# Optimization experiments

Measured on AMD Instinct MI355X. Metric: run time of the kernel, lower is better.

## Reference

```python
import jax, jax.numpy as jnp
import numpy as np

BIG = 1e10  # large finite value standing in for +inf in masked mins (grad-safe)


def setup_inputs() -> dict:
    key = jax.random.key(0)
    k1, k2, k3 = jax.random.split(key, 3)
    B, C, N = 16, 3, 4096
    x = jax.random.normal(k1, (B, C, N), dtype=jnp.float32)
    y = jax.random.normal(k2, (B, C, N), dtype=jnp.float32)
    mask = jax.random.randint(k3, (B, N), 0, 2, dtype=jnp.int32)
    return {"x": x, "y": y, "mask": mask}


def reference(x, y, mask):
    # x, y: (B, 3, N); mask: (B, N) with 1 = valid point
    xt = jnp.swapaxes(x, 1, 2)  # (B, N, 3)
    yt = jnp.swapaxes(y, 1, 2)  # (B, N, 3)
    xx = jnp.sum(xt * xt, axis=-1)  # (B, N)
    yy = jnp.sum(yt * yt, axis=-1)  # (B, N)
    # squared pairwise distances, P[b, n, m] = ||x_bn - y_bm||^2
    P = xx[:, :, None] + yy[:, None, :] - 2.0 * jnp.einsum("bnd,bmd->bnm", xt, yt)

    valid = mask.astype(bool)                 # (B, N)
    mf = mask.astype(P.dtype)                 # (B, N)
    cnt = jnp.sum(mf, axis=1)                 # (B,) number of valid points per batch

    # direction 1: for each y-point m, min over valid x-rows n; mean over valid m
    mins1 = jnp.min(jnp.where(valid[:, :, None], P, BIG), axis=1)  # (B, N)
    means1 = jnp.sum(mins1 * mf, axis=1) / cnt                      # (B,)

    # direction 2: for each x-point m, min over valid y-cols n; mean over valid m
    mins2 = jnp.min(jnp.where(valid[:, None, :], P, BIG), axis=2)  # (B, N)
    means2 = jnp.sum(mins2 * mf, axis=1) / cnt                      # (B,)

    return jnp.mean(means1) + jnp.mean(means2)
```

## Files before the change

### kernel.cpp

```cpp
#include <hip/hip_runtime.h>

typedef short bf16x8 __attribute__((ext_vector_type(8)));
typedef float f32x16 __attribute__((ext_vector_type(16)));

#define BIG_F 1e10f
constexpr int B = 16;
constexpr int N = 4096;
constexpr int ROWS = 128;
constexpr int COLS = 512;
constexpr int NRB = N / ROWS;
constexpr int NCB = N / COLS;

__device__ __forceinline__ void split(float v, unsigned& h, unsigned& l) {
    unsigned hb = __float_as_uint(v) & 0xFFFF0000u;
    h = hb >> 16;
    float r = v - __uint_as_float(hb);
    l = __float_as_uint(r) >> 16;
}

__device__ __forceinline__ float min3f(float a, float b, float c) {
    return fminf(fminf(a, b), c);
}

__device__ __forceinline__ float vmin16(f32x16 C) {
    float u0 = min3f(C[0], C[1], C[2]);
    float u1 = min3f(C[3], C[4], C[5]);
    float u2 = min3f(C[6], C[7], C[8]);
    float u3 = min3f(C[9], C[10], C[11]);
    float u4 = min3f(C[12], C[13], C[14]);
    return min3f(min3f(u0, u1, u2), fminf(u3, u4), C[15]);
}

__global__ __launch_bounds__(256) void pack_kernel(
    const float* __restrict__ x, const float* __restrict__ y,
    const int* __restrict__ mask,
    uint4* __restrict__ Apg,
    uint4* __restrict__ Bpg,
    float* __restrict__ out)
{
    const int idx = blockIdx.x * 256 + threadIdx.x;
    if (idx == 0) out[0] = 0.0f;
    const int b  = idx >> 12;
    const int pt = idx & (N - 1);
    const float* xb = x + (size_t)b * 3 * N;
    const float* yb = y + (size_t)b * 3 * N;
    const float madd = mask[b * N + pt] ? 0.0f : BIG_F;
    {
        float x0 = xb[pt], x1 = xb[N + pt], x2 = xb[2 * N + pt];
        float xx = fmaf(x2, x2, fmaf(x1, x1, x0 * x0)) + madd;
        unsigned h0, l0, h1, l1, h2, l2, xh, xl;
        split(-2.0f * x0, h0, l0);
        split(-2.0f * x1, h1, l1);
        split(-2.0f * x2, h2, l2);
        split(xx, xh, xl);
        uint4 w0 = { h0 | (h1 << 16), h2 | (h0 << 16), h1 | (h2 << 16), l0 | (l1 << 16) };
        uint4 w1 = { l2 | (l0 << 16), l1 | (l2 << 16), xh | (xl << 16), 0x3F803F80u };
        Apg[(size_t)(b * 2 + 0) * N + pt] = w0;
        Apg[(size_t)(b * 2 + 1) * N + pt] = w1;
    }
    {
        float y0 = yb[pt], y1 = yb[N + pt], y2 = yb[2 * N + pt];
        float yy = fmaf(y2, y2, fmaf(y1, y1, y0 * y0)) + madd;
        unsigned h0, l0, h1, l1, h2, l2, qh, ql;
        split(y0, h0, l0);
        split(y1, h1, l1);
        split(y2, h2, l2);
        split(yy, qh, ql);
        unsigned u0 = h0 | (h1 << 16);
        unsigned u1 = h2 | (l0 << 16);
        unsigned u2 = l1 | (l2 << 16);
        uint4 w0 = { u0, u1, u2, u0 };
        uint4 w1 = { u1, u2, 0x3F803F80u, qh | (ql << 16) };
        Bpg[(size_t)(b * 2 + 0) * N + pt] = w0;
        Bpg[(size_t)(b * 2 + 1) * N + pt] = w1;
    }
}

__global__ __launch_bounds__(256, 4) void chamfer_mfma(
    const uint4* __restrict__ Apg, const uint4* __restrict__ Bpg,
    float* __restrict__ rowpart,
    float* __restrict__ colpart)
{
    const int rb = blockIdx.x & 31;
    const int cb = blockIdx.x >> 5;
    const int b  = blockIdx.y;
    const int t  = threadIdx.x;

    __shared__ __align__(16) unsigned short Bpack[2][COLS][8];
    __shared__ float colbuf[4][COLS];

    uint4* Bl = (uint4*)&Bpack[0][0][0];
    const uint4* Bg = Bpg + (size_t)b * 2 * N + cb * COLS;
#pragma unroll
    for (int k = 0; k < 4; ++k) {
        int i = t + k * 256;
        Bl[i] = Bg[(size_t)(i >> 9) * N + (i & 511)];
    }

    const int w    = t >> 6;
    const int L    = t & 63;
    const int half = L >> 5;
    const int lc   = L & 31;

    uint4 av = Apg[(size_t)(b * 2 + half) * N + rb * ROWS + w * 32 + lc];
    bf16x8 afr = *(bf16x8*)&av;
    __syncthreads();

    const unsigned short* Bb = &Bpack[half][lc][0];

    float rm[16];
#pragma unroll
    for (int r = 0; r < 16; ++r) rm[r] = 1e30f;

    const f32x16 z16 = {0.f,0.f,0.f,0.f,0.f,0.f,0.f,0.f,
                        0.f,0.f,0.f,0.f,0.f,0.f,0.f,0.f};

#pragma unroll 1
    for (int p = 0; p < 8; ++p) {
        bf16x8 bf0 = *(const bf16x8*)(Bb + p * 512);
        bf16x8 bf1 = *(const bf16x8*)(Bb + p * 512 + 256);
        f32x16 C0 = __builtin_amdgcn_mfma_f32_32x32x16_bf16(afr, bf0, z16, 0, 0, 0);
        f32x16 C1 = __builtin_amdgcn_mfma_f32_32x32x16_bf16(afr, bf1, z16, 0, 0, 0);
#pragma unroll
        for (int r = 0; r < 16; ++r) rm[r] = min3f(rm[r], C0[r], C1[r]);
        float v0 = vmin16(C0), v1 = vmin16(C1);
        v0 = fminf(v0, __shfl_xor(v0, 32));
        v1 = fminf(v1, __shfl_xor(v1, 32));
        if (half == 0) {
            colbuf[w][p * 64 + lc]      = v0;
            colbuf[w][p * 64 + 32 + lc] = v1;
        }
    }

#pragma unroll
    for (int off = 1; off <= 16; off <<= 1)
#pragma unroll
        for (int r = 0; r < 16; ++r)
            rm[r] = fminf(rm[r], __shfl_xor(rm[r], off));
    if (lc == 0) {
        float* rp = rowpart + ((size_t)b * NCB + cb) * N + rb * ROWS + w * 32 + half * 4;
#pragma unroll
        for (int r = 0; r < 16; ++r)
            rp[(r & 3) + 8 * (r >> 2)] = rm[r];
    }

    __syncthreads();
    float* cpo = colpart + ((size_t)b * NRB + rb) * N + cb * COLS;
#pragma unroll
    for (int i = 0; i < 2; ++i) {
        int c = t + i * 256;
        float v = fminf(fminf(colbuf[0][c], colbuf[1][c]),
                        fminf(colbuf[2][c], colbuf[3][c]));
        cpo[c] = v;
    }
}

__global__ __launch_bounds__(256) void finalize_kernel(
    const int* __restrict__ mask,
    const float* __restrict__ rowpart, const float* __restrict__ colpart,
    float* __restrict__ out)
{
    const int b = blockIdx.x & 15;
    const int q = blockIdx.x >> 4;
    const int t = threadIdx.x;
    const int* mrow = mask + b * N;

    int cnt = 0;
    for (int i = t; i < N / 4; i += 256) {
        int4 mk = ((const int4*)mrow)[i];
        cnt += mk.x + mk.y + mk.z + mk.w;
    }

    const int p0 = q * 1024 + t * 4;

    const float* cp = colpart + (size_t)b * NRB * N + p0;
    float4 mn = *(const float4*)cp;
#pragma unroll 4
    for (int pb = 1; pb < NRB; ++pb) {
        float4 v = *(const float4*)(cp + (size_t)pb * N);
        mn.x = fminf(mn.x, v.x); mn.y = fminf(mn.y, v.y);
        mn.z = fminf(mn.z, v.z); mn.w = fminf(mn.w, v.w);
    }
    const float* rp = rowpart + (size_t)b * NCB * N + p0;
    float4 rn = *(const float4*)rp;
#pragma unroll
    for (int pb = 1; pb < NCB; ++pb) {
        float4 v = *(const float4*)(rp + (size_t)pb * N);
        rn.x = fminf(rn.x, v.x); rn.y = fminf(rn.y, v.y);
        rn.z = fminf(rn.z, v.z); rn.w = fminf(rn.w, v.w);
    }
    int4 mk = *(const int4*)(mrow + p0);
    float s = (mk.x ? (mn.x + rn.x) : 0.f) + (mk.y ? (mn.y + rn.y) : 0.f)
            + (mk.z ? (mn.z + rn.z) : 0.f) + (mk.w ? (mn.w + rn.w) : 0.f);

    for (int off = 32; off > 0; off >>= 1) {
        s   += __shfl_down(s, off);
        cnt += __shfl_down(cnt, off);
    }
    __shared__ float rs[4];
    __shared__ int   rc[4];
    const int wv = t >> 6;
    if ((t & 63) == 0) { rs[wv] = s; rc[wv] = cnt; }
    __syncthreads();
    if (t == 0) {
        float S = rs[0] + rs[1] + rs[2] + rs[3];
        float C = (float)(rc[0] + rc[1] + rc[2] + rc[3]);
        atomicAdd(out, (S / C) * (1.0f / 16.0f));
    }
}

extern "C" void kernel_launch(void* const* d_in, const int* in_sizes, int n_in,
                              void* d_out, int out_size, void* d_ws, size_t ws_size,
                              hipStream_t stream) {
    const float* x    = (const float*)d_in[0];
    const float* y    = (const float*)d_in[1];
    const int*   mask = (const int*)d_in[2];

    uint4* Apg     = (uint4*)d_ws;
    uint4* Bpg     = Apg + (size_t)B * 2 * N;
    float* rowpart = (float*)(Bpg + (size_t)B * 2 * N);
    float* colpart = rowpart + (size_t)B * NCB * N;

    pack_kernel<<<dim3(B * N / 256), 256, 0, stream>>>(
        x, y, mask, Apg, Bpg, (float*)d_out);
    chamfer_mfma<<<dim3(NRB * NCB, B), 256, 0, stream>>>(
        Apg, Bpg, rowpart, colpart);
    finalize_kernel<<<dim3(64), 256, 0, stream>>>(
        mask, rowpart, colpart, (float*)d_out);
}
```

Before: 97.17 us.

## Fuse pack, distance and finalize into one cooperative persistent kernel

Replaces the three kernel launches with one cooperative kernel that runs the pack, MFMA distance and finalize phases, separated by grid-wide syncs. It also makes each block reuse its staged B tile across four row blocks, and drops the cross-half shuffle by using eight colbuf slots. This is meant to cut launch overhead and redundant LDS loads of the B tile, at the cost of grid.sync latency, an extra __syncthreads per row block, and occupancy limited by the larger shared memory footprint.

```diff
diff --git a/kernel.cpp b/kernel.cpp
--- a/kernel.cpp
+++ b/kernel.cpp
@@ -1,4 +1,7 @@
 #include <hip/hip_runtime.h>
+#include <hip/hip_cooperative_groups.h>
+
+namespace cg = cooperative_groups;
 
 typedef short bf16x8 __attribute__((ext_vector_type(8)));
 typedef float f32x16 __attribute__((ext_vector_type(16)));
@@ -10,6 +13,7 @@
 constexpr int COLS = 512;
 constexpr int NRB = N / ROWS;
 constexpr int NCB = N / COLS;
+constexpr int VBLOCKS = 1024;
 
 __device__ __forceinline__ void split(float v, unsigned& h, unsigned& l) {
     unsigned hb = __float_as_uint(v) & 0xFFFF0000u;
@@ -31,181 +35,183 @@
     return min3f(min3f(u0, u1, u2), fminf(u3, u4), C[15]);
 }
 
-__global__ __launch_bounds__(256) void pack_kernel(
+__global__ __launch_bounds__(256, 4) void chamfer_all(
     const float* __restrict__ x, const float* __restrict__ y,
     const int* __restrict__ mask,
     uint4* __restrict__ Apg,
     uint4* __restrict__ Bpg,
+    float* __restrict__ rowpart,
+    float* __restrict__ colpart,
     float* __restrict__ out)
 {
-    const int idx = blockIdx.x * 256 + threadIdx.x;
-    if (idx == 0) out[0] = 0.0f;
-    const int b  = idx >> 12;
-    const int pt = idx & (N - 1);
-    const float* xb = x + (size_t)b * 3 * N;
-    const float* yb = y + (size_t)b * 3 * N;
-    const float madd = mask[b * N + pt] ? 0.0f : BIG_F;
-    {
-        float x0 = xb[pt], x1 = xb[N + pt], x2 = xb[2 * N + pt];
-        float xx = fmaf(x2, x2, fmaf(x1, x1, x0 * x0)) + madd;
-        unsigned h0, l0, h1, l1, h2, l2, xh, xl;
-        split(-2.0f * x0, h0, l0);
-        split(-2.0f * x1, h1, l1);
-        split(-2.0f * x2, h2, l2);
-        split(xx, xh, xl);
-        uint4 w0 = { h0 | (h1 << 16), h2 | (h0 << 16), h1 | (h2 << 16), l0 | (l1 << 16) };
-        uint4 w1 = { l2 | (l0 << 16), l1 | (l2 << 16), xh | (xl << 16), 0x3F803F80u };
-        Apg[(size_t)(b * 2 + 0) * N + pt] = w0;
-        Apg[(size_t)(b * 2 + 1) * N + pt] = w1;
-    }
-    {
-        float y0 = yb[pt], y1 = yb[N + pt], y2 = yb[2 * N + pt];
-        float yy = fmaf(y2, y2, fmaf(y1, y1, y0 * y0)) + madd;
-        unsigned h0, l0, h1, l1, h2, l2, qh, ql;
-        split(y0, h0, l0);
-        split(y1, h1, l1);
-        split(y2, h2, l2);
-        split(yy, qh, ql);
-        unsigned u0 = h0 | (h1 << 16);
-        unsigned u1 = h2 | (l0 << 16);
-        unsigned u2 = l1 | (l2 << 16);
-        uint4 w0 = { u0, u1, u2, u0 };
-        uint4 w1 = { u1, u2, 0x3F803F80u, qh | (ql << 16) };
-        Bpg[(size_t)(b * 2 + 0) * N + pt] = w0;
-        Bpg[(size_t)(b * 2 + 1) * N + pt] = w1;
-    }
-}
-
-__global__ __launch_bounds__(256, 4) void chamfer_mfma(
-    const uint4* __restrict__ Apg, const uint4* __restrict__ Bpg,
-    float* __restrict__ rowpart,
-    float* __restrict__ colpart)
-{
-    const int rb = blockIdx.x & 31;
-    const int cb = blockIdx.x >> 5;
-    const int b  = blockIdx.y;
-    const int t  = threadIdx.x;
+    cg::grid_group grid = cg::this_grid();
+    const int blk = blockIdx.x;
+    const int t   = threadIdx.x;
 
     __shared__ __align__(16) unsigned short Bpack[2][COLS][8];
-    __shared__ float colbuf[4][COLS];
-
-    uint4* Bl = (uint4*)&Bpack[0][0][0];
-    const uint4* Bg = Bpg + (size_t)b * 2 * N + cb * COLS;
-#pragma unroll
-    for (int k = 0; k < 4; ++k) {
-        int i = t + k * 256;
-        Bl[i] = Bg[(size_t)(i >> 9) * N + (i & 511)];
-    }
+    __shared__ float colbuf[8][COLS];
+    __shared__ float rs[4];
+    __shared__ int   rc[4];
+
+    for (int idx = blk * 256 + t; idx < B * N; idx += gridDim.x * 256) {
+        if (idx == 0) out[0] = 0.0f;
+        const int pb = idx >> 12;
+        const int pt = idx & (N - 1);
+        const float* xb = x + (size_t)pb * 3 * N;
+        const float* yb = y + (size_t)pb * 3 * N;
+        const float madd = mask[pb * N + pt] ? 0.0f : BIG_F;
+        {
+            float x0 = xb[pt], x1 = xb[N + pt], x2 = xb[2 * N + pt];
+            float xx = fmaf(x2, x2, fmaf(x1, x1, x0 * x0)) + madd;
+            unsigned h0, l0, h1, l1, h2, l2, xh, xl;
+            split(-2.0f * x0, h0, l0);
+            split(-2.0f * x1, h1, l1);
+            split(-2.0f * x2, h2, l2);
+            split(xx, xh, xl);
+            uint4 w0 = { h0 | (h1 << 16), h2 | (h0 << 16), h1 | (h2 << 16), l0 | (l1 << 16) };
+            uint4 w1 = { l2 | (l0 << 16), l1 | (l2 << 16), xh | (xl << 16), 0x3F803F80u };
+            Apg[(size_t)(pb * 2 + 0) * N + pt] = w0;
+            Apg[(size_t)(pb * 2 + 1) * N + pt] = w1;
+        }
+        {
+            float y0 = yb[pt], y1 = yb[N + pt], y2 = yb[2 * N + pt];
+            float yy = fmaf(y2, y2, fmaf(y1, y1, y0 * y0)) + madd;
+            unsigned h0, l0, h1, l1, h2, l2, qh, ql;
+            split(y0, h0, l0);
+            split(y1, h1, l1);
+            split(y2, h2, l2);
+            split(yy, qh, ql);
+            unsigned u0 = h0 | (h1 << 16);
+            unsigned u1 = h2 | (l0 << 16);
+            unsigned u2 = l1 | (l2 << 16);
+            uint4 w0 = { u0, u1, u2, u0 };
+            uint4 w1 = { u1, u2, 0x3F803F80u, qh | (ql << 16) };
+            Bpg[(size_t)(pb * 2 + 0) * N + pt] = w0;
+            Bpg[(size_t)(pb * 2 + 1) * N + pt] = w1;
+        }
+    }
+    grid.sync();
 
     const int w    = t >> 6;
     const int L    = t & 63;
     const int half = L >> 5;
     const int lc   = L & 31;
 
-    uint4 av = Apg[(size_t)(b * 2 + half) * N + rb * ROWS + w * 32 + lc];
-    bf16x8 afr = *(bf16x8*)&av;
-    __syncthreads();
-
-    const unsigned short* Bb = &Bpack[half][lc][0];
-
-    float rm[16];
-#pragma unroll
-    for (int r = 0; r < 16; ++r) rm[r] = 1e30f;
-
     const f32x16 z16 = {0.f,0.f,0.f,0.f,0.f,0.f,0.f,0.f,
                         0.f,0.f,0.f,0.f,0.f,0.f,0.f,0.f};
 
+    for (int vb = blk; vb < VBLOCKS; vb += gridDim.x) {
+        const int grp = vb >> 3;
+        const int b   = grp >> 3;
+        const int cb  = grp & 7;
+        const int sub = vb & 7;
+
+        uint4* Bl = (uint4*)&Bpack[0][0][0];
+        const uint4* Bg = Bpg + (size_t)b * 2 * N + cb * COLS;
+#pragma unroll
+        for (int k = 0; k < 4; ++k) {
+            int i = t + k * 256;
+            Bl[i] = Bg[(size_t)(i >> 9) * N + (i & 511)];
+        }
+        __syncthreads();
+
+        const unsigned short* Bb = &Bpack[half][lc][0];
+
 #pragma unroll 1
-    for (int p = 0; p < 8; ++p) {
-        bf16x8 bf0 = *(const bf16x8*)(Bb + p * 512);
-        bf16x8 bf1 = *(const bf16x8*)(Bb + p * 512 + 256);
-        f32x16 C0 = __builtin_amdgcn_mfma_f32_32x32x16_bf16(afr, bf0, z16, 0, 0, 0);
-        f32x16 C1 = __builtin_amdgcn_mfma_f32_32x32x16_bf16(afr, bf1, z16, 0, 0, 0);
-#pragma unroll
-        for (int r = 0; r < 16; ++r) rm[r] = min3f(rm[r], C0[r], C1[r]);
-        float v0 = vmin16(C0), v1 = vmin16(C1);
-        v0 = fminf(v0, __shfl_xor(v0, 32));
-        v1 = fminf(v1, __shfl_xor(v1, 32));
-        if (half == 0) {
-            colbuf[w][p * 64 + lc]      = v0;
-            colbuf[w][p * 64 + 32 + lc] = v1;
-        }
-    }
-
-#pragma unroll
-    for (int off = 1; off <= 16; off <<= 1)
-#pragma unroll
-        for (int r = 0; r < 16; ++r)
-            rm[r] = fminf(rm[r], __shfl_xor(rm[r], off));
-    if (lc == 0) {
-        float* rp = rowpart + ((size_t)b * NCB + cb) * N + rb * ROWS + w * 32 + half * 4;
-#pragma unroll
-        for (int r = 0; r < 16; ++r)
-            rp[(r & 3) + 8 * (r >> 2)] = rm[r];
-    }
-
-    __syncthreads();
-    float* cpo = colpart + ((size_t)b * NRB + rb) * N + cb * COLS;
-#pragma unroll
-    for (int i = 0; i < 2; ++i) {
-        int c = t + i * 256;
-        float v = fminf(fminf(colbuf[0][c], colbuf[1][c]),
-                        fminf(colbuf[2][c], colbuf[3][c]));
-        cpo[c] = v;
-    }
-}
-
-__global__ __launch_bounds__(256) void finalize_kernel(
-    const int* __restrict__ mask,
-    const float* __restrict__ rowpart, const float* __restrict__ colpart,
-    float* __restrict__ out)
-{
-    const int b = blockIdx.x & 15;
-    const int q = blockIdx.x >> 4;
-    const int t = threadIdx.x;
-    const int* mrow = mask + b * N;
-
-    int cnt = 0;
-    for (int i = t; i < N / 4; i += 256) {
-        int4 mk = ((const int4*)mrow)[i];
-        cnt += mk.x + mk.y + mk.z + mk.w;
-    }
-
-    const int p0 = q * 1024 + t * 4;
-
-    const float* cp = colpart + (size_t)b * NRB * N + p0;
-    float4 mn = *(const float4*)cp;
+        for (int jj = 0; jj < 4; ++jj) {
+            const int rb = sub * 4 + jj;
+            uint4 av = Apg[(size_t)(b * 2 + half) * N + rb * ROWS + w * 32 + lc];
+            bf16x8 afr = *(bf16x8*)&av;
+
+            float rm[16];
+#pragma unroll
+            for (int r = 0; r < 16; ++r) rm[r] = 1e30f;
+
+#pragma unroll 1
+            for (int p = 0; p < 8; ++p) {
+                bf16x8 bf0 = *(const bf16x8*)(Bb + p * 512);
+                bf16x8 bf1 = *(const bf16x8*)(Bb + p * 512 + 256);
+                f32x16 C0 = __builtin_amdgcn_mfma_f32_32x32x16_bf16(afr, bf0, z16, 0, 0, 0);
+                f32x16 C1 = __builtin_amdgcn_mfma_f32_32x32x16_bf16(afr, bf1, z16, 0, 0, 0);
+#pragma unroll
+                for (int r = 0; r < 16; ++r) rm[r] = min3f(rm[r], C0[r], C1[r]);
+                colbuf[w * 2 + half][p * 64 + lc]      = vmin16(C0);
+                colbuf[w * 2 + half][p * 64 + 32 + lc] = vmin16(C1);
+            }
+
+#pragma unroll
+            for (int off = 1; off <= 16; off <<= 1)
+#pragma unroll
+                for (int r = 0; r < 16; ++r)
+                    rm[r] = fminf(rm[r], __shfl_xor(rm[r], off));
+            if (lc == 0) {
+                float* rp = rowpart + ((size_t)b * NCB + cb) * N + rb * ROWS
+                          + w * 32 + half * 4;
+#pragma unroll
+                for (int r = 0; r < 16; ++r)
+                    rp[(r & 3) + 8 * (r >> 2)] = rm[r];
+            }
+
+            __syncthreads();
+            float* cpo = colpart + ((size_t)b * NRB + rb) * N + cb * COLS;
+#pragma unroll
+            for (int i = 0; i < 2; ++i) {
+                int c = t + i * 256;
+                float v = colbuf[0][c];
+#pragma unroll
+                for (int s = 1; s < 8; ++s) v = fminf(v, colbuf[s][c]);
+                cpo[c] = v;
+            }
+            __syncthreads();
+        }
+    }
+    grid.sync();
+
+    if (blk < 64) {
+        const int b = blk & 15;
+        const int q = blk >> 4;
+        const int* mrow = mask + b * N;
+
+        int cnt = 0;
+        for (int i = t; i < N / 4; i += 256) {
+            int4 mk = ((const int4*)mrow)[i];
+            cnt += mk.x + mk.y + mk.z + mk.w;
+        }
+
+        const int p0 = q * 1024 + t * 4;
+
+        const float* cp = colpart + (size_t)b * NRB * N + p0;
+        float4 mn = *(const float4*)cp;
 #pragma unroll 4
-    for (int pb = 1; pb < NRB; ++pb) {
-        float4 v = *(const float4*)(cp + (size_t)pb * N);
-        mn.x = fminf(mn.x, v.x); mn.y = fminf(mn.y, v.y);
-        mn.z = fminf(mn.z, v.z); mn.w = fminf(mn.w, v.w);
-    }
-    const float* rp = rowpart + (size_t)b * NCB * N + p0;
-    float4 rn = *(const float4*)rp;
-#pragma unroll
-    for (int pb = 1; pb < NCB; ++pb) {
-        float4 v = *(const float4*)(rp + (size_t)pb * N);
-        rn.x = fminf(rn.x, v.x); rn.y = fminf(rn.y, v.y);
-        rn.z = fminf(rn.z, v.z); rn.w = fminf(rn.w, v.w);
-    }
-    int4 mk = *(const int4*)(mrow + p0);
-    float s = (mk.x ? (mn.x + rn.x) : 0.f) + (mk.y ? (mn.y + rn.y) : 0.f)
-            + (mk.z ? (mn.z + rn.z) : 0.f) + (mk.w ? (mn.w + rn.w) : 0.f);
-
-    for (int off = 32; off > 0; off >>= 1) {
-        s   += __shfl_down(s, off);
-        cnt += __shfl_down(cnt, off);
-    }
-    __shared__ float rs[4];
-    __shared__ int   rc[4];
-    const int wv = t >> 6;
-    if ((t & 63) == 0) { rs[wv] = s; rc[wv] = cnt; }
-    __syncthreads();
-    if (t == 0) {
-        float S = rs[0] + rs[1] + rs[2] + rs[3];
-        float C = (float)(rc[0] + rc[1] + rc[2] + rc[3]);
-        atomicAdd(out, (S / C) * (1.0f / 16.0f));
+        for (int pb = 1; pb < NRB; ++pb) {
+            float4 v = *(const float4*)(cp + (size_t)pb * N);
+            mn.x = fminf(mn.x, v.x); mn.y = fminf(mn.y, v.y);
+            mn.z = fminf(mn.z, v.z); mn.w = fminf(mn.w, v.w);
+        }
+        const float* rp = rowpart + (size_t)b * NCB * N + p0;
+        float4 rn = *(const float4*)rp;
+#pragma unroll
+        for (int pb = 1; pb < NCB; ++pb) {
+            float4 v = *(const float4*)(rp + (size_t)pb * N);
+            rn.x = fminf(rn.x, v.x); rn.y = fminf(rn.y, v.y);
+            rn.z = fminf(rn.z, v.z); rn.w = fminf(rn.w, v.w);
+        }
+        int4 mk = *(const int4*)(mrow + p0);
+        float s = (mk.x ? (mn.x + rn.x) : 0.f) + (mk.y ? (mn.y + rn.y) : 0.f)
+                + (mk.z ? (mn.z + rn.z) : 0.f) + (mk.w ? (mn.w + rn.w) : 0.f);
+
+        for (int off = 32; off > 0; off >>= 1) {
+            s   += __shfl_down(s, off);
+            cnt += __shfl_down(cnt, off);
+        }
+        const int wv = t >> 6;
+        if ((t & 63) == 0) { rs[wv] = s; rc[wv] = cnt; }
+        __syncthreads();
+        if (t == 0) {
+            float S = rs[0] + rs[1] + rs[2] + rs[3];
+            float C = (float)(rc[0] + rc[1] + rc[2] + rc[3]);
+            atomicAdd(out, (S / C) * (1.0f / 16.0f));
+        }
     }
 }
 
@@ -220,11 +226,19 @@
     uint4* Bpg     = Apg + (size_t)B * 2 * N;
     float* rowpart = (float*)(Bpg + (size_t)B * 2 * N);
     float* colpart = rowpart + (size_t)B * NCB * N;
-
-    pack_kernel<<<dim3(B * N / 256), 256, 0, stream>>>(
-        x, y, mask, Apg, Bpg, (float*)d_out);
-    chamfer_mfma<<<dim3(NRB * NCB, B), 256, 0, stream>>>(
-        Apg, Bpg, rowpart, colpart);
-    finalize_kernel<<<dim3(64), 256, 0, stream>>>(
-        mask, rowpart, colpart, (float*)d_out);
-}
+    float* outp    = (float*)d_out;
+
+    static int grid = 0;
+    if (grid == 0) {
+        int occ = 0;
+        if (hipOccupancyMaxActiveBlocksPerMultiprocessor(&occ, chamfer_all, 256, 0)
+                != hipSuccess || occ < 1)
+            occ = 2;
+        grid = occ * 256;
+        if (grid > VBLOCKS) grid = VBLOCKS;
+    }
+
+    void* args[] = { (void*)&x, (void*)&y, (void*)&mask, (void*)&Apg, (void*)&Bpg,
+                     (void*)&rowpart, (void*)&colpart, (void*)&outp };
+    hipLaunchCooperativeKernel(chamfer_all, dim3(grid), dim3(256), args, 0, stream);
+}
```

New measurement: 207.2 us. 113% more time.
